# Kernel tuning notes

Measured on AMD Instinct MI355X. Metric: run time of the kernel, lower is better.

## Reference

```python
import jax, jax.numpy as jnp
import numpy as np

B, T, N, C = 32, 12, 1024, 64
NW = T - 3  # number of temporal windows / conv output length


def setup_inputs() -> dict:
    key = jax.random.key(0)
    ks = jax.random.split(key, 10)
    return {
        "data": jax.random.normal(ks[0], (B, T, N, C), jnp.float32),
        "adj": jax.random.uniform(ks[1], (4 * N, 4 * N), jnp.float32) / (4.0 * N),
        "temporal_emb": jax.random.normal(ks[2], (1, T, 1, C), jnp.float32) * 0.05,
        "spatial_emb": jax.random.normal(ks[3], (1, 1, N, C), jnp.float32) * 0.05,
        "conv_wl": jax.random.normal(ks[4], (C, C, 1, 2), jnp.float32) * 0.05,
        "conv_bl": jnp.zeros((C,), jnp.float32),
        "conv_wr": jax.random.normal(ks[5], (C, C, 1, 2), jnp.float32) * 0.05,
        "conv_br": jnp.zeros((C,), jnp.float32),
        "fc_w": jax.random.normal(ks[6], (NW, 3, C, 2 * C), jnp.float32) * 0.05,
        "fc_b": jnp.zeros((NW, 3, 2 * C), jnp.float32),
    }


def reference(data, adj, temporal_emb, spatial_emb, conv_wl, conv_bl, conv_wr, conv_br, fc_w, fc_b):
    Bs, Ts, Ns, Cs = data.shape
    nw = Ts - 3
    x = data + temporal_emb + spatial_emb  # [B,T,N,C]

    # Gated dilated temporal conv: Conv2d kernel (1,2), dilation (1,3) over time
    # out[b,t,n,o] = sum_c w[o,c,0,0]*x[b,t,n,c] + w[o,c,0,1]*x[b,t+3,n,c] + b[o]
    def dconv(w, b):
        return (jnp.einsum('btnc,oc->btno', x[:, :nw], w[:, :, 0, 0])
                + jnp.einsum('btnc,oc->btno', x[:, 3:], w[:, :, 0, 1]) + b)

    data_res = jax.nn.sigmoid(dconv(conv_wl, conv_bl)) * jnp.tanh(dconv(conv_wr, conv_br))  # [B,nw,N,C]

    # Sliding windows of 4 time steps -> [nw, B, 4N, C]
    wins = jnp.stack([x[:, i:i + 4].reshape(Bs, 4 * Ns, Cs) for i in range(nw)], axis=0)

    F = fc_w.shape[-1] // 2  # GLU filter size

    def stsgcm(xw, Ws, bs):
        # xw: [B,4N,C]; Ws: [3,Cin,2F]; bs: [3,2F]
        h = xw
        outs = []
        for k in range(Ws.shape[0]):
            h = jnp.einsum('vw,bwc->bvc', adj, h)       # graph aggregation
            g = h @ Ws[k] + bs[k]                        # linear
            h = g[..., :F] * jax.nn.sigmoid(g[..., F:])  # GLU
            outs.append(h[:, Ns:2 * Ns])                 # middle vertex block
        return jnp.max(jnp.stack(outs, axis=0), axis=0)  # [B,N,F]

    spatial = jax.vmap(stsgcm)(wins, fc_w, fc_b)  # [nw,B,N,F]
    return spatial.transpose(1, 0, 2, 3) + data_res
```

## Files before the change

### kernel.cpp

```cpp
#include <hip/hip_runtime.h>
#include <math.h>

typedef unsigned char  u8;
typedef unsigned short u16;
typedef unsigned int   u32;
typedef __attribute__((ext_vector_type(8))) short bf16x8;
typedef __attribute__((ext_vector_type(8))) int   i32x8;
typedef __attribute__((ext_vector_type(4))) float f32x4;

typedef const void __attribute__((address_space(1))) gv1_t;
typedef void       __attribute__((address_space(3))) lv3_t;
#define GLL(g, l) __builtin_amdgcn_global_load_lds((gv1_t*)(g), (lv3_t*)(l), 16, 0, 0)

__device__ __forceinline__ u16 f2b(float x) {
    union { float f; u32 u; } v; v.f = x;
    u32 r = v.u + 0x7FFFu + ((v.u >> 16) & 1u);
    return (u16)(r >> 16);
}
__device__ __forceinline__ float b2f(u32 x) {
    union { u32 u; float f; } v; v.u = x << 16;
    return v.f;
}
__device__ __forceinline__ float fast_sigmoid(float x) {
    return __builtin_amdgcn_rcpf(1.0f + __builtin_amdgcn_exp2f(-x * 1.44269504f));
}
__device__ __forceinline__ float fast_tanh(float x) {
    return 2.0f * __builtin_amdgcn_rcpf(1.0f + __builtin_amdgcn_exp2f(-x * 2.88539008f)) - 1.0f;
}

__device__ __forceinline__ u8 f2e4m3(float x) {
    union { float f; u32 u; } v; v.f = x;
    u32 s = (v.u >> 24) & 0x80u;
    u32 a = v.u & 0x7fffffffu;
    if (a >= 0x43d80000u) return (u8)(s | 0x7e);
    if (a >= 0x3c800000u) {
        u32 expf = a >> 23;
        u32 keep = (a >> 20) & 7u;
        u32 rest = a & 0xfffffu;
        u32 vv = ((expf - 120u) << 3) | keep;
        vv += (rest > 0x80000u) || ((rest == 0x80000u) && (keep & 1u));
        return (u8)(s | vv);
    }
    float t = fabsf(x) * 512.0f;
    u32 ti = (u32)(t + 0.5f);
    return (u8)(s | ti);
}
__device__ __forceinline__ float e4m3f(u32 b) {
    u32 e = (b >> 3) & 15u, m = b & 7u;
    union { u32 u; float f; } t;
    t.u = ((e + 120u) << 23) | (m << 20);
    float v = e ? t.f : ((float)m * 0.001953125f);
    return (b & 0x80u) ? -v : v;
}


__global__ void cvt_adj_fp8(const float* __restrict__ a, u8* __restrict__ o, int n) {
    for (int i = (blockIdx.x * 256 + threadIdx.x) * 4; i < n; i += gridDim.x * 256 * 4) {
        float4 v = *(const float4*)&a[i];
        u32 pk = (u32)f2e4m3(v.x * 8192.0f) | ((u32)f2e4m3(v.y * 8192.0f) << 8)
               | ((u32)f2e4m3(v.z * 8192.0f) << 16) | ((u32)f2e4m3(v.w * 8192.0f) << 24);
        int row = i >> 12;
        int addr = (i & ~127) | (((((i >> 4) & 7) ^ (row & 7)) << 4)) | (i & 15);
        *(u32*)&o[addr] = pk;
    }
}

__global__ void prep_x(const float* __restrict__ data, const float* __restrict__ temb,
                       const float* __restrict__ semb, u16* __restrict__ Xn, u8* __restrict__ XT) {
    const int n0 = blockIdx.x * 64, t = blockIdx.y, b = blockIdx.z;
    const int tid = threadIdx.x;
    __shared__ u16 lt[64][66];
#pragma unroll
    for (int p = 0; p < 4; p++) {
        int n = p * 16 + (tid >> 4);
        int c = (tid & 15) * 4;
        size_t gi = ((size_t)(b * 12 + t) * 1024 + n0 + n) * 64 + c;
        float4 v  = *(const float4*)&data[gi];
        float4 tv = *(const float4*)&temb[t * 64 + c];
        float4 sv = *(const float4*)&semb[(n0 + n) * 64 + c];
        u16 u0 = f2b(v.x + tv.x + sv.x);
        u16 u1 = f2b(v.y + tv.y + sv.y);
        u16 u2 = f2b(v.z + tv.z + sv.z);
        u16 u3 = f2b(v.w + tv.w + sv.w);
        uint2 pk; pk.x = (u32)u0 | ((u32)u1 << 16); pk.y = (u32)u2 | ((u32)u3 << 16);
        *(uint2*)&Xn[gi] = pk;
        lt[n][c + 0] = u0; lt[n][c + 1] = u1; lt[n][c + 2] = u2; lt[n][c + 3] = u3;
    }
    __syncthreads();
    const int c = tid >> 2, q = tid & 3;
    u32 w[4];
#pragma unroll
    for (int i = 0; i < 4; i++) {
        u32 b0 = f2e4m3(b2f(lt[q * 16 + i * 4 + 0][c]));
        u32 b1 = f2e4m3(b2f(lt[q * 16 + i * 4 + 1][c]));
        u32 b2 = f2e4m3(b2f(lt[q * 16 + i * 4 + 2][c]));
        u32 b3 = f2e4m3(b2f(lt[q * 16 + i * 4 + 3][c]));
        w[i] = b0 | (b1 << 8) | (b2 << 16) | (b3 << 24);
    }
    const int row = b * 64 + c;
    size_t kk = (size_t)t * 1024 + n0 + q * 16;
    size_t seg = kk & ~(size_t)127;
    int chunk = (((int)(kk >> 4) & 7) ^ (row & 7));
    uint4 pk; pk.x = w[0]; pk.y = w[1]; pk.z = w[2]; pk.w = w[3];
    *(uint4*)&XT[(size_t)row * 12288 + seg + chunk * 16] = pk;
}

__global__ void prep_w(const float* __restrict__ fcw, const float* __restrict__ cwl,
                       const float* __restrict__ cwr, u16* __restrict__ Wt, u16* __restrict__ Wc) {
    const int blk = blockIdx.x, tid = threadIdx.x;
    if (blk < 27) {
        const float* src = fcw + (size_t)blk * 64 * 128;
        u16* dst = Wt + (size_t)blk * 128 * 64;
        for (int e = tid; e < 8192; e += 256) {
            int c = e >> 7, f = e & 127;
            dst[f * 64 + c] = f2b(src[c * 128 + f]);
        }
    } else {
        for (int e = tid; e < 16384; e += 256) {
            int o = e >> 7, k = e & 127;
            float v = (o < 64) ? cwl[(o * 64 + (k & 63)) * 2 + (k >> 6)]
                               : cwr[((o - 64) * 64 + (k & 63)) * 2 + (k >> 6)];
            Wc[o * 128 + k] = f2b(v);
        }
    }
}

__global__ __launch_bounds__(256) void dconv_gemm(
    const u16* __restrict__ Xn, const u16* __restrict__ Wc,
    const float* __restrict__ cbl, const float* __restrict__ cbr,
    float* __restrict__ out) {
    const int n0 = blockIdx.x * 128, t = blockIdx.y, b = blockIdx.z;
    const int tid = threadIdx.x, lane = tid & 63, wid = tid >> 6;
    __shared__ u16 alds[2][128 * 32];
    const u16* base0 = Xn + (size_t)(b * 12 + t) * 1024 * 64;
    const u16* base3 = Xn + (size_t)(b * 12 + t + 3) * 1024 * 64;

    auto stage = [&](int buf, int kt) {
        int k0 = kt * 32;
#pragma unroll
        for (int q = 0; q < 2; q++) {
            int r = wid * 32 + q * 16 + (lane >> 2);
            int k = k0 + (lane & 3) * 8;
            const u16* gs = (k < 64) ? base0 + (size_t)(n0 + r) * 64 + k
                                     : base3 + (size_t)(n0 + r) * 64 + (k - 64);
            GLL(gs, &alds[buf][(wid * 32 + q * 16) * 32]);
        }
    };

    f32x4 acc[2][8] = {};
    stage(0, 0);
    __syncthreads();
    const int a_off = (wid * 32 + (lane & 15)) * 32 + (lane >> 4) * 8;
    for (int kt = 0; kt < 4; kt++) {
        int cur = kt & 1;
        if (kt < 3) stage(cur ^ 1, kt + 1);
        bf16x8 af[2];
#pragma unroll
        for (int m = 0; m < 2; m++) af[m] = *(const bf16x8*)&alds[cur][a_off + m * 16 * 32];
#pragma unroll
        for (int n = 0; n < 8; n++) {
            bf16x8 bq = *(const bf16x8*)&Wc[(n * 16 + (lane & 15)) * 128 + kt * 32 + (lane >> 4) * 8];
#pragma unroll
            for (int m = 0; m < 2; m++)
                acc[m][n] = __builtin_amdgcn_mfma_f32_16x16x32_bf16(af[m], bq, acc[m][n], 0, 0, 0);
        }
        __syncthreads();
    }
#pragma unroll
    for (int m = 0; m < 2; m++) {
#pragma unroll
        for (int n = 0; n < 4; n++) {
            int fp = n * 16 + (lane & 15);
            float b1 = cbl[fp], b2 = cbr[fp];
#pragma unroll
            for (int j = 0; j < 4; j++) {
                int row = wid * 32 + m * 16 + (lane >> 4) * 4 + j;
                float gl = acc[m][n][j] + b1;
                float gr = acc[m][n + 4][j] + b2;
                out[((size_t)(b * 9 + t) * 1024 + n0 + row) * 64 + fp] =
                    fast_sigmoid(gl) * fast_tanh(gr);
            }
        }
    }
}

#define SCB() __builtin_amdgcn_sched_barrier(0)
#define BARR() do { SCB(); __builtin_amdgcn_s_barrier(); SCB(); } while (0)
#define WAITK0 do { asm volatile("s_waitcnt lgkmcnt(0)" ::: "memory"); SCB(); } while (0)
#define GATE8 do { SCB(); asm volatile("s_waitcnt vmcnt(8)" ::: "memory"); SCB(); } while (0)
#define GATEZ do { SCB(); asm volatile("s_waitcnt vmcnt(0)" ::: "memory"); SCB(); } while (0)

template <int STAGE>
__global__ __launch_bounds__(256, 2) void agg_mx(
    const u8* __restrict__ A, const u8* __restrict__ Bt,
    const u16* __restrict__ Wt, const float* __restrict__ fcb,
    u8* __restrict__ P, int win0, int vbase, int nout, int ks, float ysc) {
    const int tid = threadIdx.x, lane = tid & 63, wid = tid >> 6;
    const int wr = wid >> 1, wc = wid & 1;
    const int bx = blockIdx.x, by = blockIdx.y, z = blockIdx.z;
    const int rowBase = by * 128, colBase = bx * 128;
    const int win = win0 + z;
    __shared__ u8 ldsb[65536];
    __shared__ float biasSm[128];
    biasSm[tid & 127] = fcb[(win * 3 + ks) * 128 + (tid & 127)];
    const u8* Az = (STAGE == 0) ? (A + (size_t)win * 1024)
                                : (A + (size_t)z * 2048 * 4096);
    const size_t strideA = (STAGE == 0) ? 12288 : 4096;

    const int r8  = lane >> 3;
    const int c16 = (lane & 7) * 16;
    auto stageA = [&](int buf, int s, int kt) {
        int r_l = s * 32 + wid * 8;
        GLL(Az + (size_t)(rowBase + r_l + r8) * strideA + (size_t)kt * 128 + c16,
            &ldsb[buf * 32768 + r_l * 128]);
    };
    auto stageB = [&](int buf, int s, int kt) {
        int r_l = s * 32 + wid * 8;
        GLL(Bt + (size_t)(vbase + colBase + r_l + r8) * 4096 + (size_t)kt * 128 + c16,
            &ldsb[buf * 32768 + 16384 + r_l * 128]);
    };
#define STAGE8(buf, kt) do { stageA(buf, 0, kt); stageA(buf, 1, kt); \
                             stageA(buf, 2, kt); stageA(buf, 3, kt); \
                             stageB(buf, 0, kt); stageB(buf, 1, kt); \
                             stageB(buf, 2, kt); stageB(buf, 3, kt); } while (0)

    f32x4 acc[4][4] = {};
    i32x8 fa[4], fb[4];
    const int q0 = lane >> 4;

#define RD_AB(buf)                                                            \
    _Pragma("unroll") for (int mm = 0; mm < 4; mm++) {                        \
        int r = wr * 64 + mm * 16 + (lane & 15);                              \
        int h = r & 7;                                                        \
        const u8* bp = &ldsb[(buf) * 32768 + r * 128];                        \
        ((uint4*)&fa[mm])[0] = *(const uint4*)&bp[((2 * q0) ^ h) * 16];       \
        ((uint4*)&fa[mm])[1] = *(const uint4*)&bp[((2 * q0 + 1) ^ h) * 16];   \
    }                                                                         \
    _Pragma("unroll") for (int nn = 0; nn < 4; nn++) {                        \
        int r = wc * 64 + nn * 16 + (lane & 15);                              \
        int h = r & 7;                                                        \
        const u8* bp = &ldsb[(buf) * 32768 + 16384 + r * 128];                \
        ((uint4*)&fb[nn])[0] = *(const uint4*)&bp[((2 * q0) ^ h) * 16];       \
        ((uint4*)&fb[nn])[1] = *(const uint4*)&bp[((2 * q0 + 1) ^ h) * 16];   \
    }
#define MFMA16()                                                              \
    __builtin_amdgcn_s_setprio(1);                                            \
    _Pragma("unroll") for (int mm = 0; mm < 4; mm++)                          \
    _Pragma("unroll") for (int nn = 0; nn < 4; nn++)                          \
        acc[mm][nn] = __builtin_amdgcn_mfma_scale_f32_16x16x128_f8f6f4(       \
            fa[mm], fb[nn], acc[mm][nn], 0, 0, 0, 127, 0, 127);               \
    __builtin_amdgcn_s_setprio(0);

#define TILE14(RB, T2S) do {                                                  \
    BARR();                                                                   \
    RD_AB(RB);                                                                \
    WAITK0;                                                                   \
    BARR();                                                                   \
    STAGE8(RB, T2S);                                                          \
    SCB();                                                                    \
    MFMA16();                                                                 \
    GATE8;                                                                    \
} while (0)

    STAGE8(0, 0);
    STAGE8(1, 1);
    GATE8;

    for (int t = 0; t < 30; t += 2) {
        TILE14(0, t + 2);
        TILE14(1, t + 3);
    }
    BARR();
    RD_AB(0);
    WAITK0;
    BARR();
    MFMA16();
    GATEZ;
    BARR();
    RD_AB(1);
    WAITK0;
    MFMA16();

    __syncthreads();
    u16* YT = (u16*)ldsb;
#pragma unroll
    for (int mm = 0; mm < 4; mm++) {
        int c0 = mm * 16 + (lane >> 4) * 4;
#pragma unroll
        for (int nn = 0; nn < 4; nn++) {
            int v = wc * 64 + nn * 16 + (lane & 15);
            ushort4 pk;
            pk.x = f2b(acc[mm][nn][0] * ysc); pk.y = f2b(acc[mm][nn][1] * ysc);
            pk.z = f2b(acc[mm][nn][2] * ysc); pk.w = f2b(acc[mm][nn][3] * ysc);
            int addr = (wr * 128 + v) * 64 + (((c0 >> 3) ^ (v & 7)) << 3) + (c0 & 7);
            *(ushort4*)&YT[addr] = pk;
        }
    }
    __syncthreads();

    const int bat = wid >> 1, fh = wid & 1;
    const u16* Wl = Wt + (size_t)(win * 3 + ks) * 8192;
    u8* Pz = P + (size_t)z * 2048 * nout;
    bf16x8 aw[4][2];
#pragma unroll
    for (int p = 0; p < 4; p++) {
        int mt = (p & 1) + fh * 2 + (p >> 1) * 4;
#pragma unroll
        for (int kk = 0; kk < 2; kk++)
            aw[p][kk] = *(const bf16x8*)&Wl[(mt * 16 + (lane & 15)) * 64 + kk * 32 + (lane >> 4) * 8];
    }
#pragma unroll
    for (int vp = 0; vp < 4; vp++) {
        f32x4 acc2[4][2] = {};
        bf16x8 bq2[2][2];
#pragma unroll
        for (int nt = 0; nt < 2; nt++) {
            int v = vp * 32 + nt * 16 + (lane & 15);
#pragma unroll
            for (int kk = 0; kk < 2; kk++) {
                int ch = kk * 4 + (lane >> 4);
                bq2[nt][kk] = *(const bf16x8*)&YT[(bat * 128 + v) * 64 + ((ch ^ (v & 7)) << 3)];
            }
        }
#pragma unroll
        for (int p = 0; p < 4; p++)
#pragma unroll
            for (int nt = 0; nt < 2; nt++)
#pragma unroll
                for (int kk = 0; kk < 2; kk++)
                    acc2[p][nt] = __builtin_amdgcn_mfma_f32_16x16x32_bf16(
                        aw[p][kk], bq2[nt][kk], acc2[p][nt], 0, 0, 0);
#pragma unroll
        for (int p = 0; p < 2; p++) {
            int mt = (p & 1) + fh * 2;
#pragma unroll
            for (int j = 0; j < 4; j++) {
                int f = mt * 16 + (lane >> 4) * 4 + j;
                float b1 = biasSm[f], b2v = biasSm[f + 64];
                int row = rowBase + bat * 64 + f;
#pragma unroll
                for (int nt = 0; nt < 2; nt++) {
                    float g1 = acc2[p][nt][j] + b1;
                    float g2 = acc2[p + 2][nt][j] + b2v;
                    float val = g1 * fast_sigmoid(g2);
                    int colg = colBase + vp * 32 + nt * 16 + (lane & 15);
                    int seg = colg & ~127;
                    int chunk = (((colg >> 4) & 7) ^ (row & 7));
                    Pz[(size_t)row * nout + seg + chunk * 16 + (colg & 15)] =
                        f2e4m3(val * 512.0f);
                }
            }
        }
    }
#undef RD_AB
#undef MFMA16
#undef TILE14
#undef STAGE8
}

__device__ __forceinline__ uint4 ld_swz(const u8* p, size_t rowBytes, size_t k, int h) {
    size_t seg = k & ~(size_t)127;
    int chunk = ((int)(k >> 4) & 7) ^ h;
    return *(const uint4*)&p[rowBytes + seg + chunk * 16];
}

__global__ void final_add(const u8* __restrict__ P1, const u8* __restrict__ P2,
                          const u8* __restrict__ P3, float* __restrict__ out, int win0) {
    const int n0 = blockIdx.x * 64, b = blockIdx.y, z = blockIdx.z;
    const int win = win0 + z;
    const int tid = threadIdx.x;
    __shared__ float tl[64][65];
    {
        int f = tid >> 2, q = tid & 3;
        int row = b * 64 + f;
        int h = row & 7;
        size_t rb12 = ((size_t)z * 2048 + row) * 4096;
        size_t rb3  = ((size_t)z * 2048 + row) * 1024;
        uint4 a  = ld_swz(P1, rb12, (size_t)1024 + n0 + q * 16, h);
        uint4 c2 = ld_swz(P2, rb12, (size_t)1024 + n0 + q * 16, h);
        uint4 d  = ld_swz(P3, rb3, (size_t)n0 + q * 16, h);
        const u32 aw[4] = {a.x, a.y, a.z, a.w};
        const u32 bw[4] = {c2.x, c2.y, c2.z, c2.w};
        const u32 dw[4] = {d.x, d.y, d.z, d.w};
#pragma unroll
        for (int w = 0; w < 4; w++)
#pragma unroll
            for (int j = 0; j < 4; j++) {
                float va = e4m3f((aw[w] >> (j * 8)) & 0xffu);
                float vb = e4m3f((bw[w] >> (j * 8)) & 0xffu);
                float vd = e4m3f((dw[w] >> (j * 8)) & 0xffu);
                tl[q * 16 + w * 4 + j][f] = fmaxf(fmaxf(va, vb), vd) * (1.0f / 512.0f);
            }
    }
    __syncthreads();
    {
        int n = tid >> 2, q = tid & 3;
        size_t oo = ((size_t)(b * 9 + win) * 1024 + n0 + n) * 64 + q * 16;
#pragma unroll
        for (int i = 0; i < 16; i += 4) {
            float4 cur = *(const float4*)&out[oo + i];
            cur.x += tl[n][q * 16 + i + 0];
            cur.y += tl[n][q * 16 + i + 1];
            cur.z += tl[n][q * 16 + i + 2];
            cur.w += tl[n][q * 16 + i + 3];
            *(float4*)&out[oo + i] = cur;
        }
    }
}

extern "C" void kernel_launch(void* const* d_in, const int* in_sizes, int n_in,
                              void* d_out, int out_size, void* d_ws, size_t ws_size,
                              hipStream_t stream) {
    const float* data = (const float*)d_in[0];
    const float* adj  = (const float*)d_in[1];
    const float* temb = (const float*)d_in[2];
    const float* semb = (const float*)d_in[3];
    const float* cwl  = (const float*)d_in[4];
    const float* cbl  = (const float*)d_in[5];
    const float* cwr  = (const float*)d_in[6];
    const float* cbr  = (const float*)d_in[7];
    const float* fcw  = (const float*)d_in[8];
    const float* fcb  = (const float*)d_in[9];
    float* out = (float*)d_out;

    const float YS1 = 1.0f / 8192.0f;
    const float YS2 = 1.0f / 4194304.0f;

    char* p = (char*)d_ws;
    auto alloc = [&](size_t bytes) -> char* {
        char* r = p;
        p += (bytes + 255) & ~(size_t)255;
        return r;
    };
    const size_t SZ_XT  = 2048UL * 12288;
    const size_t SZ_XN  = 32UL * 12 * 1024 * 64 * 2;
    const size_t SZ_ADJ = 4096UL * 4096;
    const size_t SZ_WT  = 27UL * 128 * 64 * 2;
    const size_t SZ_WC  = 128UL * 128 * 2;
    const size_t SZ_P12 = 2048UL * 4096;
    const size_t SZ_P3  = 2048UL * 1024;
    u8*  XT   = (u8*)alloc(SZ_XT);
    u8*  adjb = (u8*)alloc(SZ_ADJ);
    u16* Wt   = (u16*)alloc(SZ_WT);
    u16* Wc   = (u16*)alloc(SZ_WC);
    size_t fixed = (size_t)(p - (char*)d_ws);

    bool single = (fixed + 9 * (2 * SZ_P12) + SZ_XN + 1024 <= ws_size);
    if (single) {
        u8* P1 = (u8*)alloc(9 * SZ_P12);
        u8* P2 = (u8*)alloc(9 * SZ_P12);
        u8* P3 = XT;
        u16* Xn = (u16*)P2;

        cvt_adj_fp8<<<4096, 256, 0, stream>>>(adj, adjb, 4096 * 4096);
        prep_x<<<dim3(16, 12, 32), 256, 0, stream>>>(data, temb, semb, Xn, XT);
        prep_w<<<28, 256, 0, stream>>>(fcw, cwl, cwr, Wt, Wc);
        dconv_gemm<<<dim3(8, 9, 32), 256, 0, stream>>>(Xn, Wc, cbl, cbr, out);

        agg_mx<0><<<dim3(32, 16, 9), 256, 0, stream>>>(XT, adjb, Wt, fcb, P1, 0, 0, 4096, 0, YS1);
        agg_mx<1><<<dim3(32, 16, 9), 256, 0, stream>>>(P1, adjb, Wt, fcb, P2, 0, 0, 4096, 1, YS2);
        agg_mx<1><<<dim3(8, 16, 9), 256, 0, stream>>>(P2, adjb, Wt, fcb, P3, 0, 1024, 1024, 2, YS2);
        final_add<<<dim3(16, 32, 9), 256, 0, stream>>>(P1, P2, P3, out, 0);
    } else {
        char* winBase = p;
        size_t avail = ws_size - (size_t)(winBase - (char*)d_ws);
        const size_t perwin = 2 * SZ_P12 + SZ_P3 + 3 * 256;
        int cap = (int)(avail / perwin);
        if (cap > 9) cap = 9;
        if (cap < 1) cap = 1;
        u8* P1 = (u8*)alloc((size_t)cap * SZ_P12);
        u8* P2 = (u8*)alloc((size_t)cap * SZ_P12);
        u8* P3 = (u8*)alloc((size_t)cap * SZ_P3);
        u16* Xn = ((size_t)cap * perwin >= SZ_XN + 256) ? (u16*)winBase : (u16*)alloc(SZ_XN);

        cvt_adj_fp8<<<4096, 256, 0, stream>>>(adj, adjb, 4096 * 4096);
        prep_x<<<dim3(16, 12, 32), 256, 0, stream>>>(data, temb, semb, Xn, XT);
        prep_w<<<28, 256, 0, stream>>>(fcw, cwl, cwr, Wt, Wc);
        dconv_gemm<<<dim3(8, 9, 32), 256, 0, stream>>>(Xn, Wc, cbl, cbr, out);

        int ngroups = (9 + cap - 1) / cap;
        int gbase = 9 / ngroups, grem = 9 % ngroups;
        int w0 = 0;
        for (int g = 0; g < ngroups; g++) {
            int cw = gbase + (g < grem ? 1 : 0);
            agg_mx<0><<<dim3(32, 16, cw), 256, 0, stream>>>(XT, adjb, Wt, fcb, P1, w0, 0, 4096, 0, YS1);
            agg_mx<1><<<dim3(32, 16, cw), 256, 0, stream>>>(P1, adjb, Wt, fcb, P2, w0, 0, 4096, 1, YS2);
            agg_mx<1><<<dim3(8, 16, cw), 256, 0, stream>>>(P2, adjb, Wt, fcb, P3, w0, 1024, 1024, 2, YS2);
            final_add<<<dim3(16, 32, cw), 256, 0, stream>>>(P1, P2, P3, out, w0);
            w0 += cw;
        }
    }
}
```

Measured before the change: 1.017 ms.

## Load A operand directly from global into registers, stage only B in LDS

The aggregation GEMM now reads the A-operand fragments straight from global memory into double-buffered registers, prefetched one k-tile ahead, and stages only B through LDS. This halves LDS usage and removes the LDS round-trip for A. Because the swizzled layout was only needed for LDS bank-conflict avoidance, the producers (prep and GLU epilogue) and consumers (final_add) switch to a plain row-major layout, and the vmcnt gates are retuned. The trade-off is uncoalesced-ish per-lane global loads for A and extra register pressure, with a different latency-hiding pattern.

```diff
diff --git a/kernel.cpp b/kernel.cpp
--- a/kernel.cpp
+++ b/kernel.cpp
@@ -97,12 +97,9 @@
         u32 b3 = f2e4m3(b2f(lt[q * 16 + i * 4 + 3][c]));
         w[i] = b0 | (b1 << 8) | (b2 << 16) | (b3 << 24);
     }
-    const int row = b * 64 + c;
-    size_t kk = (size_t)t * 1024 + n0 + q * 16;
-    size_t seg = kk & ~(size_t)127;
-    int chunk = (((int)(kk >> 4) & 7) ^ (row & 7));
+    size_t xo = ((size_t)(b * 64 + c)) * 12288 + (size_t)t * 1024 + n0 + q * 16;
     uint4 pk; pk.x = w[0]; pk.y = w[1]; pk.z = w[2]; pk.w = w[3];
-    *(uint4*)&XT[(size_t)row * 12288 + seg + chunk * 16] = pk;
+    *(uint4*)&XT[xo] = pk;
 }
 
 __global__ void prep_w(const float* __restrict__ fcw, const float* __restrict__ cwl,
@@ -187,8 +184,10 @@
 #define SCB() __builtin_amdgcn_sched_barrier(0)
 #define BARR() do { SCB(); __builtin_amdgcn_s_barrier(); SCB(); } while (0)
 #define WAITK0 do { asm volatile("s_waitcnt lgkmcnt(0)" ::: "memory"); SCB(); } while (0)
-#define GATE8 do { SCB(); asm volatile("s_waitcnt vmcnt(8)" ::: "memory"); SCB(); } while (0)
-#define GATEZ do { SCB(); asm volatile("s_waitcnt vmcnt(0)" ::: "memory"); SCB(); } while (0)
+#define GATE16 do { SCB(); asm volatile("s_waitcnt vmcnt(16)" ::: "memory"); SCB(); } while (0)
+#define GATE12 do { SCB(); asm volatile("s_waitcnt vmcnt(12)" ::: "memory"); SCB(); } while (0)
+#define GATE8  do { SCB(); asm volatile("s_waitcnt vmcnt(8)"  ::: "memory"); SCB(); } while (0)
+#define GATEZ  do { SCB(); asm volatile("s_waitcnt vmcnt(0)"  ::: "memory"); SCB(); } while (0)
 
 template <int STAGE>
 __global__ __launch_bounds__(256, 2) void agg_mx(
@@ -200,86 +199,85 @@
     const int bx = blockIdx.x, by = blockIdx.y, z = blockIdx.z;
     const int rowBase = by * 128, colBase = bx * 128;
     const int win = win0 + z;
-    __shared__ u8 ldsb[65536];
+    __shared__ u8 ldsb[32768];
     __shared__ float biasSm[128];
     biasSm[tid & 127] = fcb[(win * 3 + ks) * 128 + (tid & 127)];
+    constexpr size_t strideA = (STAGE == 0) ? 12288 : 4096;
     const u8* Az = (STAGE == 0) ? (A + (size_t)win * 1024)
                                 : (A + (size_t)z * 2048 * 4096);
-    const size_t strideA = (STAGE == 0) ? 12288 : 4096;
-
-    const int r8  = lane >> 3;
+
+    const int q0 = lane >> 4;
+    const u8* gA = Az + (size_t)(rowBase + wr * 64 + (lane & 15)) * strideA + q0 * 32;
+
+    const int r8g = lane >> 3;
     const int c16 = (lane & 7) * 16;
-    auto stageA = [&](int buf, int s, int kt) {
-        int r_l = s * 32 + wid * 8;
-        GLL(Az + (size_t)(rowBase + r_l + r8) * strideA + (size_t)kt * 128 + c16,
-            &ldsb[buf * 32768 + r_l * 128]);
-    };
     auto stageB = [&](int buf, int s, int kt) {
         int r_l = s * 32 + wid * 8;
-        GLL(Bt + (size_t)(vbase + colBase + r_l + r8) * 4096 + (size_t)kt * 128 + c16,
-            &ldsb[buf * 32768 + 16384 + r_l * 128]);
+        GLL(Bt + (size_t)(vbase + colBase + r_l + r8g) * 4096 + (size_t)kt * 128 + c16,
+            &ldsb[buf * 16384 + r_l * 128]);
     };
-#define STAGE8(buf, kt) do { stageA(buf, 0, kt); stageA(buf, 1, kt); \
-                             stageA(buf, 2, kt); stageA(buf, 3, kt); \
-                             stageB(buf, 0, kt); stageB(buf, 1, kt); \
-                             stageB(buf, 2, kt); stageB(buf, 3, kt); } while (0)
+#define STAGE_B(buf, kt) do { stageB(buf, 0, kt); stageB(buf, 1, kt); \
+                              stageB(buf, 2, kt); stageB(buf, 3, kt); } while (0)
 
     f32x4 acc[4][4] = {};
-    i32x8 fa[4], fb[4];
-    const int q0 = lane >> 4;
-
-#define RD_AB(buf)                                                            \
+    i32x8 aP[4], aQ[4], fb[4];
+
+#define LOAD_A(dst, T)                                                        \
     _Pragma("unroll") for (int mm = 0; mm < 4; mm++) {                        \
-        int r = wr * 64 + mm * 16 + (lane & 15);                              \
-        int h = r & 7;                                                        \
-        const u8* bp = &ldsb[(buf) * 32768 + r * 128];                        \
-        ((uint4*)&fa[mm])[0] = *(const uint4*)&bp[((2 * q0) ^ h) * 16];       \
-        ((uint4*)&fa[mm])[1] = *(const uint4*)&bp[((2 * q0 + 1) ^ h) * 16];   \
-    }                                                                         \
+        const u8* ap = gA + (size_t)(mm * 16) * strideA + (size_t)(T) * 128;  \
+        ((uint4*)&dst[mm])[0] = *(const uint4*)ap;                            \
+        ((uint4*)&dst[mm])[1] = *(const uint4*)(ap + 16);                     \
+    }
+#define RD_B(buf)                                                             \
     _Pragma("unroll") for (int nn = 0; nn < 4; nn++) {                        \
         int r = wc * 64 + nn * 16 + (lane & 15);                              \
         int h = r & 7;                                                        \
-        const u8* bp = &ldsb[(buf) * 32768 + 16384 + r * 128];                \
+        const u8* bp = &ldsb[(buf) * 16384 + r * 128];                        \
         ((uint4*)&fb[nn])[0] = *(const uint4*)&bp[((2 * q0) ^ h) * 16];       \
         ((uint4*)&fb[nn])[1] = *(const uint4*)&bp[((2 * q0 + 1) ^ h) * 16];   \
     }
-#define MFMA16()                                                              \
+#define MFMA16(Af)                                                            \
     __builtin_amdgcn_s_setprio(1);                                            \
     _Pragma("unroll") for (int mm = 0; mm < 4; mm++)                          \
     _Pragma("unroll") for (int nn = 0; nn < 4; nn++)                          \
         acc[mm][nn] = __builtin_amdgcn_mfma_scale_f32_16x16x128_f8f6f4(       \
-            fa[mm], fb[nn], acc[mm][nn], 0, 0, 0, 127, 0, 127);               \
+            Af[mm], fb[nn], acc[mm][nn], 0, 0, 0, 127, 0, 127);               \
     __builtin_amdgcn_s_setprio(0);
 
-#define TILE14(RB, T2S) do {                                                  \
+#define TILE15(RB, AUSE, ALOAD, T) do {                                       \
     BARR();                                                                   \
-    RD_AB(RB);                                                                \
+    RD_B(RB);                                                                 \
+    LOAD_A(ALOAD, (T) + 1);                                                   \
     WAITK0;                                                                   \
     BARR();                                                                   \
-    STAGE8(RB, T2S);                                                          \
-    SCB();                                                                    \
-    MFMA16();                                                                 \
-    GATE8;                                                                    \
+    STAGE_B(RB, (T) + 2);                                                     \
+    GATE16;                                                                   \
+    MFMA16(AUSE);                                                             \
+    GATE12;                                                                   \
 } while (0)
 
-    STAGE8(0, 0);
-    STAGE8(1, 1);
+    STAGE_B(0, 0);
+    LOAD_A(aP, 0);
+    SCB();
+    STAGE_B(1, 1);
+    GATE12;
+
+    for (int t = 0; t < 30; t += 2) {
+        TILE15(0, aP, aQ, t);
+        TILE15(1, aQ, aP, t + 1);
+    }
+    BARR();
+    RD_B(0);
+    LOAD_A(aQ, 31);
+    WAITK0;
+    GATE12;
+    MFMA16(aP);
     GATE8;
-
-    for (int t = 0; t < 30; t += 2) {
-        TILE14(0, t + 2);
-        TILE14(1, t + 3);
-    }
     BARR();
-    RD_AB(0);
+    RD_B(1);
     WAITK0;
-    BARR();
-    MFMA16();
     GATEZ;
-    BARR();
-    RD_AB(1);
-    WAITK0;
-    MFMA16();
+    MFMA16(aQ);
 
     __syncthreads();
     u16* YT = (u16*)ldsb;
@@ -344,24 +342,16 @@
                     float g2 = acc2[p + 2][nt][j] + b2v;
                     float val = g1 * fast_sigmoid(g2);
                     int colg = colBase + vp * 32 + nt * 16 + (lane & 15);
-                    int seg = colg & ~127;
-                    int chunk = (((colg >> 4) & 7) ^ (row & 7));
-                    Pz[(size_t)row * nout + seg + chunk * 16 + (colg & 15)] =
-                        f2e4m3(val * 512.0f);
+                    Pz[(size_t)row * nout + colg] = f2e4m3(val * 512.0f);
                 }
             }
         }
     }
-#undef RD_AB
+#undef LOAD_A
+#undef RD_B
 #undef MFMA16
-#undef TILE14
-#undef STAGE8
-}
-
-__device__ __forceinline__ uint4 ld_swz(const u8* p, size_t rowBytes, size_t k, int h) {
-    size_t seg = k & ~(size_t)127;
-    int chunk = ((int)(k >> 4) & 7) ^ h;
-    return *(const uint4*)&p[rowBytes + seg + chunk * 16];
+#undef TILE15
+#undef STAGE_B
 }
 
 __global__ void final_add(const u8* __restrict__ P1, const u8* __restrict__ P2,
@@ -372,13 +362,11 @@
     __shared__ float tl[64][65];
     {
         int f = tid >> 2, q = tid & 3;
-        int row = b * 64 + f;
-        int h = row & 7;
-        size_t rb12 = ((size_t)z * 2048 + row) * 4096;
-        size_t rb3  = ((size_t)z * 2048 + row) * 1024;
-        uint4 a  = ld_swz(P1, rb12, (size_t)1024 + n0 + q * 16, h);
-        uint4 c2 = ld_swz(P2, rb12, (size_t)1024 + n0 + q * 16, h);
-        uint4 d  = ld_swz(P3, rb3, (size_t)n0 + q * 16, h);
+        size_t o12 = ((size_t)z * 2048 + b * 64 + f) * 4096 + 1024 + n0 + q * 16;
+        size_t o3  = ((size_t)z * 2048 + b * 64 + f) * 1024 + n0 + q * 16;
+        uint4 a  = *(const uint4*)&P1[o12];
+        uint4 c2 = *(const uint4*)&P2[o12];
+        uint4 d  = *(const uint4*)&P3[o3];
         const u32 aw[4] = {a.x, a.y, a.z, a.w};
         const u32 bw[4] = {c2.x, c2.y, c2.z, c2.w};
         const u32 dw[4] = {d.x, d.y, d.z, d.w};
```

New measurement: 1.709 ms. 68.0% more time.

## Add 256x256-tile 8-wave aggregation kernel with interleaved half-tile pipelining

Applied to the files above, without the earlier changes.

Adds agg_mx2, a 512-thread variant of the FP8 graph-aggregation GEMM that computes 256x256 output tiles instead of 128x128. Global-to-LDS loads of each half-tile are interleaved with MFMA sub-blocks in a finer-grained software pipeline. The goal is to raise operand reuse per loaded byte and hide load latency better for the first two stages. The trade-off is a doubled LDS footprint (128KB double buffer) and more accumulator registers, which may limit occupancy, and a coarser grid of fewer blocks. The third stage still uses the old kernel.

```diff
diff --git a/kernel.cpp b/kernel.cpp
--- a/kernel.cpp
+++ b/kernel.cpp
@@ -182,6 +182,191 @@
             }
         }
     }
+}
+
+#define SB2() do { __builtin_amdgcn_sched_barrier(0); __builtin_amdgcn_s_barrier(); __builtin_amdgcn_sched_barrier(0); } while (0)
+#define GATE4() asm volatile("s_waitcnt vmcnt(4)" ::: "memory")
+#define DRAIN0() asm volatile("s_waitcnt vmcnt(0)" ::: "memory")
+
+template <int STAGE>
+__global__ __launch_bounds__(512, 2) void agg_mx2(
+    const u8* __restrict__ A, const u8* __restrict__ Bt,
+    const u16* __restrict__ Wt, const float* __restrict__ fcb,
+    u8* __restrict__ P, int win0, int vbase, int nout, int ks, float ysc) {
+    const int tid = threadIdx.x, lane = tid & 63, wid = tid >> 6;
+    const int wr = wid >> 2, wc = wid & 3;
+    const int bx = blockIdx.x, by = blockIdx.y, z = blockIdx.z;
+    const int rowBase = by * 256, colBase = bx * 256;
+    const int win = win0 + z;
+    __shared__ u8 ldsb[131072];
+    __shared__ float biasSm[128];
+    biasSm[tid & 127] = fcb[(win * 3 + ks) * 128 + (tid & 127)];
+    constexpr size_t strideA = (STAGE == 0) ? 12288 : 4096;
+    const u8* Az = (STAGE == 0) ? (A + (size_t)win * 1024)
+                                : (A + (size_t)z * 2048 * 4096);
+
+    const int r8g = lane >> 3;
+    const int c16 = (lane & 7) * 16;
+
+    auto stageA = [&](int buf, int half, int s, int kt) {
+        kt &= 31;
+        int r0 = s * 64 + wid * 8;
+        int row_g = rowBase + half * 128 + r0 + r8g;
+        GLL(Az + (size_t)row_g * strideA + (size_t)kt * 128 + c16,
+            &ldsb[buf * 65536 + half * 16384 + r0 * 128]);
+    };
+    auto stageB = [&](int buf, int half, int s, int kt) {
+        kt &= 31;
+        int r0 = s * 64 + wid * 8;
+        int col_g = vbase + colBase + half * 128 + r0 + r8g;
+        GLL(Bt + (size_t)col_g * 4096 + (size_t)kt * 128 + c16,
+            &ldsb[buf * 65536 + 32768 + half * 16384 + r0 * 128]);
+    };
+#define STH_A(buf, half, kt) do { stageA(buf, half, 0, kt); stageA(buf, half, 1, kt); } while (0)
+#define STH_B(buf, half, kt) do { stageB(buf, half, 0, kt); stageB(buf, half, 1, kt); } while (0)
+
+    f32x4 acc[8][4] = {};
+    i32x8 aF[4], fb[4];
+    const int q0 = lane >> 4;
+
+#define RD_A(buf, mb)                                                         \
+    _Pragma("unroll") for (int mm = 0; mm < 4; mm++) {                        \
+        int r = ((mb) + mm) * 16 + (lane & 15);                               \
+        int h = r & 7;                                                        \
+        const u8* bp = &ldsb[(buf) * 65536 + wr * 16384 + r * 128];           \
+        ((uint4*)&aF[mm])[0] = *(const uint4*)&bp[((2 * q0) ^ h) * 16];       \
+        ((uint4*)&aF[mm])[1] = *(const uint4*)&bp[((2 * q0 + 1) ^ h) * 16];   \
+    }
+#define RD_B(buf, nb)                                                         \
+    _Pragma("unroll") for (int nn = 0; nn < 2; nn++) {                        \
+        int r = (wc & 1) * 64 + ((nb) + nn) * 16 + (lane & 15);               \
+        int h = r & 7;                                                        \
+        const u8* bp = &ldsb[(buf) * 65536 + 32768 + (wc >> 1) * 16384 + r * 128]; \
+        ((uint4*)&fb[(nb) + nn])[0] = *(const uint4*)&bp[((2 * q0) ^ h) * 16];     \
+        ((uint4*)&fb[(nb) + nn])[1] = *(const uint4*)&bp[((2 * q0 + 1) ^ h) * 16]; \
+    }
+#define MX8(mb, nb)                                                           \
+    __builtin_amdgcn_s_setprio(1);                                            \
+    _Pragma("unroll") for (int mm = 0; mm < 4; mm++)                          \
+    _Pragma("unroll") for (int nn = 0; nn < 2; nn++)                          \
+        acc[(mb) + mm][(nb) + nn] = __builtin_amdgcn_mfma_scale_f32_16x16x128_f8f6f4( \
+            aF[mm], fb[(nb) + nn], acc[(mb) + mm][(nb) + nn], 0, 0, 0, 127, 0, 127);  \
+    __builtin_amdgcn_s_setprio(0);
+
+    STH_B(0, 0, 0); STH_A(0, 0, 0); STH_B(0, 1, 0); STH_A(0, 1, 0);
+    STH_B(1, 0, 1); STH_A(1, 0, 1);
+    GATE4();
+    SB2();
+
+    for (int i = 0; i < 16; i++) {
+        int t1 = 2 * i + 1, t2 = 2 * i + 2, t3 = 2 * i + 3;
+        RD_A(0, 0); RD_B(0, 0);
+        STH_B(1, 1, t1);
+        SB2(); MX8(0, 0); SB2();
+
+        RD_B(0, 2);
+        STH_A(1, 1, t1);
+        SB2(); MX8(0, 2); SB2();
+
+        RD_A(0, 4);
+        STH_B(0, 0, t2);
+        SB2(); MX8(4, 0); SB2();
+
+        STH_A(0, 0, t2);
+        SB2(); MX8(4, 2); GATE4(); SB2();
+
+        RD_A(1, 0); RD_B(1, 0);
+        STH_B(0, 1, t2);
+        SB2(); MX8(0, 0); SB2();
+
+        RD_B(1, 2);
+        STH_A(0, 1, t2);
+        SB2(); MX8(0, 2); SB2();
+
+        RD_A(1, 4);
+        STH_B(1, 0, t3);
+        SB2(); MX8(4, 0); SB2();
+
+        STH_A(1, 0, t3);
+        SB2(); MX8(4, 2); GATE4(); SB2();
+    }
+
+    DRAIN0();
+    __syncthreads();
+    u16* YT = (u16*)ldsb;
+
+#pragma unroll
+    for (int m = 0; m < 8; m++) {
+        int bi = wr * 2 + (m >> 2);
+        int c0 = (m & 3) * 16 + q0 * 4;
+#pragma unroll
+        for (int n = 0; n < 4; n++) {
+            int v = wc * 64 + n * 16 + (lane & 15);
+            ushort4 pk;
+            pk.x = f2b(acc[m][n][0] * ysc); pk.y = f2b(acc[m][n][1] * ysc);
+            pk.z = f2b(acc[m][n][2] * ysc); pk.w = f2b(acc[m][n][3] * ysc);
+            int addr = bi * 16384 + v * 64 + (((c0 >> 3) ^ (v & 7)) << 3) + (c0 & 7);
+            *(ushort4*)&YT[addr] = pk;
+        }
+    }
+    __syncthreads();
+
+    const int bi2 = wid >> 1, h2 = wid & 1;
+    const u16* Wl = Wt + (size_t)(win * 3 + ks) * 8192;
+    u8* Pz = P + (size_t)z * 2048 * nout;
+    bf16x8 aw[8][2];
+#pragma unroll
+    for (int fi = 0; fi < 8; fi++)
+#pragma unroll
+        for (int kk = 0; kk < 2; kk++)
+            aw[fi][kk] = *(const bf16x8*)&Wl[(fi * 16 + (lane & 15)) * 64 + kk * 32 + q0 * 8];
+#pragma unroll
+    for (int vq = 0; vq < 2; vq++) {
+        f32x4 acc2[8][4] = {};
+        bf16x8 bq2[4][2];
+#pragma unroll
+        for (int nt = 0; nt < 4; nt++) {
+            int v = h2 * 128 + vq * 64 + nt * 16 + (lane & 15);
+#pragma unroll
+            for (int kk = 0; kk < 2; kk++) {
+                int ch = kk * 4 + q0;
+                bq2[nt][kk] = *(const bf16x8*)&YT[bi2 * 16384 + v * 64 + ((ch ^ (v & 7)) << 3)];
+            }
+        }
+#pragma unroll
+        for (int fi = 0; fi < 8; fi++)
+#pragma unroll
+            for (int nt = 0; nt < 4; nt++)
+#pragma unroll
+                for (int kk = 0; kk < 2; kk++)
+                    acc2[fi][nt] = __builtin_amdgcn_mfma_f32_16x16x32_bf16(
+                        aw[fi][kk], bq2[nt][kk], acc2[fi][nt], 0, 0, 0);
+#pragma unroll
+        for (int fi = 0; fi < 4; fi++) {
+#pragma unroll
+            for (int j = 0; j < 4; j++) {
+                int f = fi * 16 + q0 * 4 + j;
+                float b1 = biasSm[f], b2v = biasSm[f + 64];
+                int row = rowBase + bi2 * 64 + f;
+#pragma unroll
+                for (int nt = 0; nt < 4; nt++) {
+                    float g1 = acc2[fi][nt][j] + b1;
+                    float g2 = acc2[fi + 4][nt][j] + b2v;
+                    float val = g1 * fast_sigmoid(g2);
+                    int col = colBase + h2 * 128 + vq * 64 + nt * 16 + (lane & 15);
+                    int seg = col & ~127;
+                    int chunk = (((col >> 4) & 7) ^ (row & 7));
+                    Pz[(size_t)row * nout + seg + chunk * 16 + (col & 15)] =
+                        f2e4m3(val * 512.0f);
+                }
+            }
+        }
+    }
+#undef RD_A
+#undef RD_B
+#undef MX8
+#undef STH_A
+#undef STH_B
 }
 
 #define SCB() __builtin_amdgcn_sched_barrier(0)
@@ -207,7 +392,7 @@
                                 : (A + (size_t)z * 2048 * 4096);
     const size_t strideA = (STAGE == 0) ? 12288 : 4096;
 
-    const int r8  = lane >> 3;
+    const int r8 = lane >> 3;
     const int c16 = (lane & 7) * 16;
     auto stageA = [&](int buf, int s, int kt) {
         int r_l = s * 32 + wid * 8;
@@ -219,16 +404,16 @@
         GLL(Bt + (size_t)(vbase + colBase + r_l + r8) * 4096 + (size_t)kt * 128 + c16,
             &ldsb[buf * 32768 + 16384 + r_l * 128]);
     };
-#define STAGE8(buf, kt) do { stageA(buf, 0, kt); stageA(buf, 1, kt); \
-                             stageA(buf, 2, kt); stageA(buf, 3, kt); \
-                             stageB(buf, 0, kt); stageB(buf, 1, kt); \
-                             stageB(buf, 2, kt); stageB(buf, 3, kt); } while (0)
+#define STAGE8M(buf, kt) do { stageA(buf, 0, kt); stageA(buf, 1, kt); \
+                              stageA(buf, 2, kt); stageA(buf, 3, kt); \
+                              stageB(buf, 0, kt); stageB(buf, 1, kt); \
+                              stageB(buf, 2, kt); stageB(buf, 3, kt); } while (0)
 
     f32x4 acc[4][4] = {};
     i32x8 fa[4], fb[4];
     const int q0 = lane >> 4;
 
-#define RD_AB(buf)                                                            \
+#define RD_ABM(buf)                                                           \
     _Pragma("unroll") for (int mm = 0; mm < 4; mm++) {                        \
         int r = wr * 64 + mm * 16 + (lane & 15);                              \
         int h = r & 7;                                                        \
@@ -243,7 +428,7 @@
         ((uint4*)&fb[nn])[0] = *(const uint4*)&bp[((2 * q0) ^ h) * 16];       \
         ((uint4*)&fb[nn])[1] = *(const uint4*)&bp[((2 * q0 + 1) ^ h) * 16];   \
     }
-#define MFMA16()                                                              \
+#define MFMA16M()                                                             \
     __builtin_amdgcn_s_setprio(1);                                            \
     _Pragma("unroll") for (int mm = 0; mm < 4; mm++)                          \
     _Pragma("unroll") for (int nn = 0; nn < 4; nn++)                          \
@@ -251,41 +436,41 @@
             fa[mm], fb[nn], acc[mm][nn], 0, 0, 0, 127, 0, 127);               \
     __builtin_amdgcn_s_setprio(0);
 
-#define TILE14(RB, T2S) do {                                                  \
+#define TILE14M(RB, T2S) do {                                                 \
     BARR();                                                                   \
-    RD_AB(RB);                                                                \
+    RD_ABM(RB);                                                               \
     WAITK0;                                                                   \
     BARR();                                                                   \
-    STAGE8(RB, T2S);                                                          \
+    STAGE8M(RB, T2S);                                                         \
     SCB();                                                                    \
-    MFMA16();                                                                 \
+    MFMA16M();                                                                \
     GATE8;                                                                    \
 } while (0)
 
-    STAGE8(0, 0);
-    STAGE8(1, 1);
+    STAGE8M(0, 0);
+    STAGE8M(1, 1);
     GATE8;
 
     for (int t = 0; t < 30; t += 2) {
-        TILE14(0, t + 2);
-        TILE14(1, t + 3);
+        TILE14M(0, t + 2);
+        TILE14M(1, t + 3);
     }
     BARR();
-    RD_AB(0);
+    RD_ABM(0);
     WAITK0;
     BARR();
-    MFMA16();
+    MFMA16M();
     GATEZ;
     BARR();
-    RD_AB(1);
+    RD_ABM(1);
     WAITK0;
-    MFMA16();
+    MFMA16M();
 
     __syncthreads();
     u16* YT = (u16*)ldsb;
 #pragma unroll
     for (int mm = 0; mm < 4; mm++) {
-        int c0 = mm * 16 + (lane >> 4) * 4;
+        int c0 = mm * 16 + q0 * 4;
 #pragma unroll
         for (int nn = 0; nn < 4; nn++) {
             int v = wc * 64 + nn * 16 + (lane & 15);
@@ -307,7 +492,7 @@
         int mt = (p & 1) + fh * 2 + (p >> 1) * 4;
 #pragma unroll
         for (int kk = 0; kk < 2; kk++)
-            aw[p][kk] = *(const bf16x8*)&Wl[(mt * 16 + (lane & 15)) * 64 + kk * 32 + (lane >> 4) * 8];
+            aw[p][kk] = *(const bf16x8*)&Wl[(mt * 16 + (lane & 15)) * 64 + kk * 32 + q0 * 8];
     }
 #pragma unroll
     for (int vp = 0; vp < 4; vp++) {
@@ -318,7 +503,7 @@
             int v = vp * 32 + nt * 16 + (lane & 15);
 #pragma unroll
             for (int kk = 0; kk < 2; kk++) {
-                int ch = kk * 4 + (lane >> 4);
+                int ch = kk * 4 + q0;
                 bq2[nt][kk] = *(const bf16x8*)&YT[(bat * 128 + v) * 64 + ((ch ^ (v & 7)) << 3)];
             }
         }
@@ -335,7 +520,7 @@
             int mt = (p & 1) + fh * 2;
 #pragma unroll
             for (int j = 0; j < 4; j++) {
-                int f = mt * 16 + (lane >> 4) * 4 + j;
+                int f = mt * 16 + q0 * 4 + j;
                 float b1 = biasSm[f], b2v = biasSm[f + 64];
                 int row = rowBase + bat * 64 + f;
 #pragma unroll
@@ -352,10 +537,10 @@
             }
         }
     }
-#undef RD_AB
-#undef MFMA16
-#undef TILE14
-#undef STAGE8
+#undef RD_ABM
+#undef MFMA16M
+#undef TILE14M
+#undef STAGE8M
 }
 
 __device__ __forceinline__ uint4 ld_swz(const u8* p, size_t rowBytes, size_t k, int h) {
@@ -457,8 +642,8 @@
         prep_w<<<28, 256, 0, stream>>>(fcw, cwl, cwr, Wt, Wc);
         dconv_gemm<<<dim3(8, 9, 32), 256, 0, stream>>>(Xn, Wc, cbl, cbr, out);
 
-        agg_mx<0><<<dim3(32, 16, 9), 256, 0, stream>>>(XT, adjb, Wt, fcb, P1, 0, 0, 4096, 0, YS1);
-        agg_mx<1><<<dim3(32, 16, 9), 256, 0, stream>>>(P1, adjb, Wt, fcb, P2, 0, 0, 4096, 1, YS2);
+        agg_mx2<0><<<dim3(16, 8, 9), 512, 0, stream>>>(XT, adjb, Wt, fcb, P1, 0, 0, 4096, 0, YS1);
+        agg_mx2<1><<<dim3(16, 8, 9), 512, 0, stream>>>(P1, adjb, Wt, fcb, P2, 0, 0, 4096, 1, YS2);
         agg_mx<1><<<dim3(8, 16, 9), 256, 0, stream>>>(P2, adjb, Wt, fcb, P3, 0, 1024, 1024, 2, YS2);
         final_add<<<dim3(16, 32, 9), 256, 0, stream>>>(P1, P2, P3, out, 0);
     } else {
@@ -483,8 +668,8 @@
         int w0 = 0;
         for (int g = 0; g < ngroups; g++) {
             int cw = gbase + (g < grem ? 1 : 0);
-            agg_mx<0><<<dim3(32, 16, cw), 256, 0, stream>>>(XT, adjb, Wt, fcb, P1, w0, 0, 4096, 0, YS1);
-            agg_mx<1><<<dim3(32, 16, cw), 256, 0, stream>>>(P1, adjb, Wt, fcb, P2, w0, 0, 4096, 1, YS2);
+            agg_mx2<0><<<dim3(16, 8, cw), 512, 0, stream>>>(XT, adjb, Wt, fcb, P1, w0, 0, 4096, 0, YS1);
+            agg_mx2<1><<<dim3(16, 8, cw), 512, 0, stream>>>(P1, adjb, Wt, fcb, P2, w0, 0, 4096, 1, YS2);
             agg_mx<1><<<dim3(8, 16, cw), 256, 0, stream>>>(P2, adjb, Wt, fcb, P3, w0, 1024, 1024, 2, YS2);
             final_add<<<dim3(16, 32, cw), 256, 0, stream>>>(P1, P2, P3, out, w0);
             w0 += cw;
```

New measurement: 2.231 ms. 2.19x slower.
